# Optimization experiments

Measured on AMD Instinct MI355X. Metric: run time of the kernel, lower is better.

The kernel has to match this reference:

```python
import jax, jax.numpy as jnp
import numpy as np

DIM = 128
HEADS = 4
HEAD_DIM = DIM // HEADS
SCALE = HEAD_DIM ** -0.5


def setup_inputs() -> dict:
    k0 = jax.random.key(0)
    ks = jax.random.split(k0, 20)
    B, N, Hq, Wq_, Hk, Wk_ = 1, 6, 100, 100, 16, 44
    s = 0.02
    return {
        "query": jax.random.normal(ks[0], (B, DIM, Hq, Wq_), jnp.float32),
        "key": jax.random.normal(ks[1], (B, N, DIM, Hk, Wk_), jnp.float32),
        "value": jax.random.normal(ks[2], (B, N, DIM, Hk, Wk_), jnp.float32),
        "depth": jax.random.uniform(ks[3], (B, N, 1, Hk, Wk_), jnp.float32),
        "depth_confidence": jax.random.uniform(ks[4], (B, N, 1, Hk, Wk_), jnp.float32),
        "skip": jax.random.normal(ks[5], (B, DIM, Hq, Wq_), jnp.float32),
        "Wq": jax.random.normal(ks[6], (DIM, DIM), jnp.float32) * s,
        "bq": jnp.zeros((DIM,), jnp.float32),
        "Wk": jax.random.normal(ks[7], (DIM, DIM), jnp.float32) * s,
        "bk": jnp.zeros((DIM,), jnp.float32),
        "Wv": jax.random.normal(ks[8], (DIM, DIM), jnp.float32) * s,
        "bv": jnp.zeros((DIM,), jnp.float32),
        "Wo": jax.random.normal(ks[9], (DIM, DIM), jnp.float32) * s,
        "bo": jnp.zeros((DIM,), jnp.float32),
        "dw1": jax.random.normal(ks[10], (DIM // 4, 1), jnp.float32) * s,  # 1x1 conv: 1 -> dim/4
        "db1": jnp.zeros((DIM // 4,), jnp.float32),
        "dw2": jax.random.normal(ks[11], (HEADS, DIM // 4), jnp.float32) * s,  # 1x1 conv: dim/4 -> heads
        "db2": jnp.zeros((HEADS,), jnp.float32),
    }


def _forward(query, key, value, depth, depth_confidence, skip,
             Wq, bq, Wk, bk, Wv, bv, Wo, bo, dw1, db1, dw2, db2):
    B, dim, Hq, Wq_ = query.shape
    N, Hk, Wk_ = key.shape[1], key.shape[3], key.shape[4]
    Lq, Lk = Hq * Wq_, N * Hk * Wk_

    # b d h w -> b (h w) d
    qf = jnp.transpose(query, (0, 2, 3, 1)).reshape(B, Lq, dim)
    # b n d h w -> b (n h w) d
    kf = jnp.transpose(key, (0, 1, 3, 4, 2)).reshape(B, Lk, dim)
    vf = jnp.transpose(value, (0, 1, 3, 4, 2)).reshape(B, Lk, dim)

    def heads(x, W, b):  # (B,L,dim) -> (B,H,L,hd)
        y = x @ W.T + b
        return jnp.transpose(y.reshape(B, -1, HEADS, HEAD_DIM), (0, 2, 1, 3))

    Q = heads(qf, Wq, bq)
    K = heads(kf, Wk, bk)
    V = heads(vf, Wv, bv)

    attn = jnp.einsum('bhqd,bhkd->bhqk', Q, K) * SCALE  # (B,H,Lq,Lk)

    # depth weighting bias: two 1x1 convs + softmax over heads channel
    d = jnp.transpose(depth, (0, 1, 3, 4, 2))  # (B,N,Hk,Wk,1)
    t = jax.nn.relu(d @ dw1.T + db1)            # (B,N,Hk,Wk,dim/4)
    t = t @ dw2.T + db2                          # (B,N,Hk,Wk,heads)
    dw = jax.nn.softmax(t, axis=-1)
    conf = jnp.transpose(depth_confidence, (0, 1, 3, 4, 2))  # (B,N,Hk,Wk,1)
    cw = conf * dw                               # (B,N,Hk,Wk,heads)
    bias = 0.1 * jnp.transpose(cw, (0, 4, 1, 2, 3)).reshape(B, HEADS, 1, Lk)

    attn = jax.nn.softmax(attn + bias, axis=-1)
    out = jnp.einsum('bhqk,bhkd->bhqd', attn, V)             # (B,H,Lq,hd)
    out = jnp.transpose(out, (0, 2, 1, 3)).reshape(B, Lq, dim)
    out = out @ Wo.T + bo
    out = jnp.transpose(out.reshape(B, Hq, Wq_, dim), (0, 3, 1, 2))
    return out + skip


def reference(query, key, value, depth, depth_confidence, skip,
              Wq, bq, Wk, bk, Wv, bv, Wo, bo, dw1, db1, dw2, db2):
    return _forward(query, key, value, depth, depth_confidence, skip,
                    Wq, bq, Wk, bk, Wv, bv, Wo, bo, dw1, db1, dw2, db2)
```

## Files before the change

kernel.cpp:

```cpp
#include <hip/hip_runtime.h>
#include <stdint.h>

#define LQ 10000
#define LK 4224
#define NQB 313
#define SCALE 0.17677669529663687f
#define LOG2E 1.44269504088896341f
#define SCALE2 (SCALE * LOG2E)

typedef __bf16 bf16x8 __attribute__((ext_vector_type(8)));
typedef __bf16 bf16x4 __attribute__((ext_vector_type(4)));
typedef float  f32x4  __attribute__((ext_vector_type(4)));
typedef unsigned short u16x4 __attribute__((ext_vector_type(4)));

__device__ __forceinline__ unsigned short f2b(float f) {
  union { float f; unsigned u; } v; v.f = f;
  unsigned r = v.u + 0x7fffu + ((v.u >> 16) & 1u);
  return (unsigned short)(r >> 16);
}

__global__ void misc_kernel(
    const float* __restrict__ depth, const float* __restrict__ conf,
    const float* __restrict__ dw1, const float* __restrict__ db1,
    const float* __restrict__ dw2, const float* __restrict__ db2,
    const float* __restrict__ Wq, const float* __restrict__ Wk,
    const float* __restrict__ Wv, const float* __restrict__ Wo,
    float* __restrict__ biasArr,
    unsigned short* __restrict__ Wqb, unsigned short* __restrict__ Wkb,
    unsigned short* __restrict__ Wvb, unsigned short* __restrict__ Wob) {
  int b = blockIdx.x, t = threadIdx.x;
  if (b < 256) {
    int i = b * 256 + t;
    int m = i >> 14, j = i & 16383;
    const float* src = (m == 0) ? Wq : (m == 1) ? Wk : (m == 2) ? Wv : Wo;
    unsigned short* dst = (m == 0) ? Wqb : (m == 1) ? Wkb : (m == 2) ? Wvb : Wob;
    dst[j] = f2b(src[j]);
    return;
  }
  int k = (b - 256) * 256 + t;
  if (k >= LK) return;
  float d = depth[k], c = conf[k];
  float t2[4];
#pragma unroll
  for (int hh = 0; hh < 4; ++hh) t2[hh] = db2[hh];
  for (int cc = 0; cc < 32; ++cc) {
    float t1 = fmaxf(fmaf(d, dw1[cc], db1[cc]), 0.f);
#pragma unroll
    for (int hh = 0; hh < 4; ++hh) t2[hh] = fmaf(t1, dw2[hh * 32 + cc], t2[hh]);
  }
  float mx = fmaxf(fmaxf(t2[0], t2[1]), fmaxf(t2[2], t2[3]));
  float e[4], s = 0.f;
#pragma unroll
  for (int hh = 0; hh < 4; ++hh) { e[hh] = __expf(t2[hh] - mx); s += e[hh]; }
  float f = 0.1f * c / s * LOG2E;
#pragma unroll
  for (int hh = 0; hh < 4; ++hh) biasArr[hh * LK + k] = f * e[hh];
}

__global__ __launch_bounds__(256) void proj_kernel(
    const float* __restrict__ query, const float* __restrict__ key,
    const float* __restrict__ value,
    const unsigned short* __restrict__ Wqb, const float* __restrict__ bq,
    const unsigned short* __restrict__ Wkb, const float* __restrict__ bk,
    const unsigned short* __restrict__ Wvb, const float* __restrict__ bv,
    unsigned short* __restrict__ Qb, unsigned short* __restrict__ Kb,
    unsigned short* __restrict__ Vt) {
  __shared__ __align__(16) unsigned short Xb[64][136];
  int t = threadIdx.x;
  int bid = blockIdx.x;
  int isQ = (bid < 157);
  int kvid = bid - 157;
  int isV = (kvid >= 66);
  if (isV) kvid -= 66;

  const unsigned short* Wb = isQ ? Wqb : (isV ? Wvb : Wkb);
  const float* bb = isQ ? bq : (isV ? bv : bk);

  if (isQ) {
    int l0 = bid * 64;
#pragma unroll
    for (int i = 0; i < 32; ++i) {
      int e = t + 256 * i;
      int d = e >> 6, c = e & 63;
      int l = l0 + c;
      Xb[c][d] = f2b(l < LQ ? query[(size_t)d * LQ + l] : 0.f);
    }
  } else {
    const float* X = isV ? value : key;
    int k0 = kvid * 64;
    int n = k0 / 704, p0 = k0 % 704;
    const float* Xn = X + (size_t)n * 128 * 704 + p0;
#pragma unroll
    for (int i = 0; i < 32; ++i) {
      int e = t + 256 * i;
      int d = e >> 6, c = e & 63;
      Xb[c][d] = f2b(Xn[(size_t)d * 704 + c]);
    }
  }
  __syncthreads();
  int wv = t >> 6, lane = t & 63, lm = lane & 15, lg = lane >> 4;
  const f32x4 zf = {0.f, 0.f, 0.f, 0.f};
  bf16x8 af[4];
#pragma unroll
  for (int kk = 0; kk < 4; ++kk)
    af[kk] = *(const bf16x8*)&Xb[wv * 16 + lm][kk * 32 + lg * 8];
  f32x4 acc[8] = {zf, zf, zf, zf, zf, zf, zf, zf};
#pragma unroll
  for (int kk = 0; kk < 4; ++kk)
#pragma unroll
    for (int ni = 0; ni < 8; ++ni) {
      bf16x8 bfr = *(const bf16x8*)(Wb + (size_t)(ni * 16 + lm) * 128 + kk * 32 + lg * 8);
      acc[ni] = __builtin_amdgcn_mfma_f32_16x16x32_bf16(af[kk], bfr, acc[ni], 0, 0, 0);
    }
  if (isQ) {
    int l0 = bid * 64;
#pragma unroll
    for (int ni = 0; ni < 8; ++ni)
#pragma unroll
      for (int r = 0; r < 4; ++r) {
        int l = l0 + wv * 16 + lg * 4 + r;
        int dout = ni * 16 + lm;
        Qb[(size_t)l * 128 + dout] = f2b((acc[ni][r] + bb[dout]) * SCALE2);
      }
  } else if (!isV) {
    int k0 = kvid * 64;
#pragma unroll
    for (int ni = 0; ni < 8; ++ni)
#pragma unroll
      for (int r = 0; r < 4; ++r) {
        int k = k0 + wv * 16 + lg * 4 + r;
        int dout = ni * 16 + lm;
        Kb[(size_t)k * 128 + dout] = f2b(acc[ni][r] + bb[dout]);
      }
  } else {
    int k0 = kvid * 64;
#pragma unroll
    for (int ni = 0; ni < 8; ++ni)
#pragma unroll
      for (int r = 0; r < 4; ++r) {
        int k = k0 + wv * 16 + lg * 4 + r;
        int dout = ni * 16 + lm;
        Vt[(size_t)dout * LK + k] = f2b(acc[ni][r] + bb[dout]);
      }
  }
}

__global__ __launch_bounds__(256) void attn_part_kernel(
    const unsigned short* __restrict__ Qb, const unsigned short* __restrict__ Kb,
    const unsigned short* __restrict__ Vt, const float* __restrict__ biasArr,
    float* __restrict__ Opart, float* __restrict__ Ml, int tpc, int C) {
  __shared__ __align__(16) unsigned short P_lds[4][32][64];
  int t = threadIdx.x;
  int wv = t >> 6;
  int qb = blockIdx.x * 4 + wv;
  if (qb >= NQB) return;
  int h = blockIdx.y, c = blockIdx.z;
  int lane = t & 63, lm = lane & 15, lg = lane >> 4;
  const f32x4 zf = {0.f, 0.f, 0.f, 0.f};

  bf16x8 qf[2];
#pragma unroll
  for (int mi = 0; mi < 2; ++mi)
    qf[mi] = *(const bf16x8*)(Qb + (size_t)(qb * 32 + mi * 16 + lm) * 128 + h * 32 + lg * 8);

  f32x4 acc[2][2] = {{zf, zf}, {zf, zf}};
  float lrun[2] = {0.f, 0.f};

  const float* bias_h = biasArr + h * LK;
  const unsigned short* Kh = Kb + h * 32;
  const unsigned short* Vh = Vt + (size_t)h * 32 * LK;

  int wr_half = (lg & 1) * 4;
  int swz = lm & 7;

  int kb_end = c * tpc + tpc;
  for (int kb = c * tpc; kb < kb_end; ++kb) {
    int k0 = kb * 64;
    bf16x8 kf[4];
#pragma unroll
    for (int ni = 0; ni < 4; ++ni)
      kf[ni] = *(const bf16x8*)(Kh + (size_t)(k0 + ni * 16 + lm) * 128 + lg * 8);
    f32x4 bvv[4];
#pragma unroll
    for (int ni = 0; ni < 4; ++ni)
      bvv[ni] = *(const f32x4*)(bias_h + k0 + ni * 16 + lg * 4);

#pragma unroll
    for (int mi = 0; mi < 2; ++mi) {
      f32x4 S[4];
#pragma unroll
      for (int ni = 0; ni < 4; ++ni)
        S[ni] = __builtin_amdgcn_mfma_f32_16x16x32_bf16(kf[ni], qf[mi], zf, 0, 0, 0);
      float ps[4];
#pragma unroll
      for (int ni = 0; ni < 4; ++ni) {
        bf16x4 pk;
        float p0 = exp2f(S[ni][0] + bvv[ni][0]);
        float p1 = exp2f(S[ni][1] + bvv[ni][1]);
        float p2 = exp2f(S[ni][2] + bvv[ni][2]);
        float p3 = exp2f(S[ni][3] + bvv[ni][3]);
        pk[0] = (__bf16)p0; pk[1] = (__bf16)p1;
        pk[2] = (__bf16)p2; pk[3] = (__bf16)p3;
        ps[ni] = (p0 + p1) + (p2 + p3);
        int chunk = (2 * ni + (lg >> 1)) ^ swz;
        *(bf16x4*)&P_lds[wv][mi * 16 + lm][chunk * 8 + wr_half] = pk;
      }
      float psum = (ps[0] + ps[1]) + (ps[2] + ps[3]);
      psum += __shfl_xor(psum, 16);
      psum += __shfl_xor(psum, 32);
      lrun[mi] += psum;
    }
    asm volatile("" ::: "memory");
    __builtin_amdgcn_sched_barrier(0);
    bf16x8 pa[2][2], vfr[2][2];
#pragma unroll
    for (int mi = 0; mi < 2; ++mi)
#pragma unroll
      for (int kk = 0; kk < 2; ++kk) {
        int chunk = (4 * kk + lg) ^ swz;
        pa[mi][kk] = *(const bf16x8*)&P_lds[wv][mi * 16 + lm][chunk * 8];
      }
#pragma unroll
    for (int kk = 0; kk < 2; ++kk)
#pragma unroll
      for (int nd = 0; nd < 2; ++nd)
        vfr[kk][nd] = *(const bf16x8*)(Vh + (size_t)(nd * 16 + lm) * LK + k0 + kk * 32 + lg * 8);
#pragma unroll
    for (int mi = 0; mi < 2; ++mi)
#pragma unroll
      for (int nd = 0; nd < 2; ++nd)
#pragma unroll
        for (int kk = 0; kk < 2; ++kk)
          acc[mi][nd] = __builtin_amdgcn_mfma_f32_16x16x32_bf16(pa[mi][kk], vfr[kk][nd], acc[mi][nd], 0, 0, 0);
    asm volatile("" ::: "memory");
    __builtin_amdgcn_sched_barrier(0);
  }
  size_t pbase = (size_t)(qb * 4 + h) * C + c;
  float* Op = Opart + pbase * 1024;
#pragma unroll
  for (int mi = 0; mi < 2; ++mi)
#pragma unroll
    for (int nd = 0; nd < 2; ++nd)
#pragma unroll
      for (int r = 0; r < 4; ++r)
        Op[(mi * 16 + lg * 4 + r) * 32 + nd * 16 + lm] = acc[mi][nd][r];
  if (lane < 16) {
    float* MlB = Ml + pbase * 64;
#pragma unroll
    for (int mi = 0; mi < 2; ++mi)
      MlB[mi * 16 + lm] = lrun[mi];
  }
}

__global__ __launch_bounds__(256) void epi_kernel(
    const float* __restrict__ Opart, const float* __restrict__ Ml,
    const unsigned short* __restrict__ Wob, const float* __restrict__ bo,
    const float* __restrict__ skip, float* __restrict__ out, int C) {
  __shared__ __align__(16) unsigned short ObT[64][136];
  __shared__ float wls[4][32];
  int t = threadIdx.x, wv = t >> 6, lane = t & 63;
  int bx = blockIdx.x, l0 = bx * 64;
  int h = wv;

#pragma unroll
  for (int s = 0; s < 2; ++s) {
    int qb = bx * 2 + s;
    if (qb < NQB) {
      size_t base = (size_t)(qb * 4 + h) * C;
      if (lane < 32) {
        float lt = 0.f;
        for (int c = 0; c < C; ++c)
          lt += Ml[(base + c) * 64 + lane];
        wls[wv][lane] = 1.f / lt;
      }
      asm volatile("" ::: "memory");
      __builtin_amdgcn_sched_barrier(0);
      const float* Op = Opart + base * 1024;
#pragma unroll
      for (int j = 0; j < 4; ++j) {
        int q = j * 8 + (lane >> 3);
        int d = (lane & 7) * 4;
        f32x4 accv = {0.f, 0.f, 0.f, 0.f};
        for (int c = 0; c < C; ++c) {
          f32x4 v = *(const f32x4*)(Op + c * 1024 + j * 256 + lane * 4);
#pragma unroll
          for (int i = 0; i < 4; ++i) accv[i] += v[i];
        }
        float linv = wls[wv][q];
        u16x4 o4;
#pragma unroll
        for (int i = 0; i < 4; ++i) o4[i] = f2b(accv[i] * linv);
        *(u16x4*)&ObT[s * 32 + q][h * 32 + d] = o4;
      }
    } else {
#pragma unroll
      for (int j = 0; j < 4; ++j) {
        int q = j * 8 + (lane >> 3);
        int d = (lane & 7) * 4;
        u16x4 z = {0, 0, 0, 0};
        *(u16x4*)&ObT[s * 32 + q][h * 32 + d] = z;
      }
    }
  }
  __syncthreads();

  int lm = lane & 15, lg = lane >> 4;
  const f32x4 zf = {0.f, 0.f, 0.f, 0.f};
  bf16x8 af[2][4];
#pragma unroll
  for (int mi = 0; mi < 2; ++mi)
#pragma unroll
    for (int kk = 0; kk < 4; ++kk)
      af[mi][kk] = *(const bf16x8*)(Wob + (size_t)(wv * 32 + mi * 16 + lm) * 128 + kk * 32 + lg * 8);
  f32x4 acc[2][4] = {{zf, zf, zf, zf}, {zf, zf, zf, zf}};
#pragma unroll
  for (int kk = 0; kk < 4; ++kk) {
    bf16x8 bfr[4];
#pragma unroll
    for (int ni = 0; ni < 4; ++ni)
      bfr[ni] = *(const bf16x8*)&ObT[ni * 16 + lm][kk * 32 + lg * 8];
#pragma unroll
    for (int mi = 0; mi < 2; ++mi)
#pragma unroll
      for (int ni = 0; ni < 4; ++ni)
        acc[mi][ni] = __builtin_amdgcn_mfma_f32_16x16x32_bf16(af[mi][kk], bfr[ni], acc[mi][ni], 0, 0, 0);
  }
#pragma unroll
  for (int mi = 0; mi < 2; ++mi)
#pragma unroll
    for (int r = 0; r < 4; ++r) {
      int dout = wv * 32 + mi * 16 + lg * 4 + r;
      float bb = bo[dout];
#pragma unroll
      for (int ni = 0; ni < 4; ++ni) {
        int l = l0 + ni * 16 + lm;
        if (l < LQ)
          out[(size_t)dout * LQ + l] = acc[mi][ni][r] + bb + skip[(size_t)dout * LQ + l];
      }
    }
}

extern "C" void kernel_launch(void* const* d_in, const int* in_sizes, int n_in,
                              void* d_out, int out_size, void* d_ws, size_t ws_size,
                              hipStream_t stream) {
  const float* query = (const float*)d_in[0];
  const float* key   = (const float*)d_in[1];
  const float* value = (const float*)d_in[2];
  const float* depth = (const float*)d_in[3];
  const float* conf  = (const float*)d_in[4];
  const float* skip  = (const float*)d_in[5];
  const float* Wq = (const float*)d_in[6];   const float* bq = (const float*)d_in[7];
  const float* Wk = (const float*)d_in[8];   const float* bk = (const float*)d_in[9];
  const float* Wv = (const float*)d_in[10];  const float* bv = (const float*)d_in[11];
  const float* Wo = (const float*)d_in[12];  const float* bo = (const float*)d_in[13];
  const float* dw1 = (const float*)d_in[14]; const float* db1 = (const float*)d_in[15];
  const float* dw2 = (const float*)d_in[16]; const float* db2 = (const float*)d_in[17];
  float* out = (float*)d_out;
  char* ws = (char*)d_ws;

  unsigned short* Qb   = (unsigned short*)(ws + 0);
  unsigned short* Kb   = (unsigned short*)(ws + 2572288);
  unsigned short* Vt   = (unsigned short*)(ws + 3653632);
  float*          bias = (float*)        (ws + 4734976);
  unsigned short* Wqb  = (unsigned short*)(ws + 4802560);
  unsigned short* Wkb  = (unsigned short*)(ws + 4835328);
  unsigned short* Wvb  = (unsigned short*)(ws + 4868096);
  unsigned short* Wob  = (unsigned short*)(ws + 4900864);
  const size_t splitOff = 7505920;

  int C = 1;
  {
    const int cand[4] = {6, 3, 2, 1};
    for (int i = 0; i < 4; ++i) {
      size_t need = splitOff + (size_t)NQB * 4 * cand[i] * (4096 + 256);
      if (ws_size >= need) { C = cand[i]; break; }
    }
  }
  int tpc = 66 / C;
  float* Opart = (float*)(ws + splitOff);
  float* Ml    = (float*)(ws + splitOff + (size_t)NQB * 4 * C * 4096);

  hipLaunchKernelGGL(misc_kernel, dim3(273), dim3(256), 0, stream,
                     depth, conf, dw1, db1, dw2, db2, Wq, Wk, Wv, Wo,
                     bias, Wqb, Wkb, Wvb, Wob);
  hipLaunchKernelGGL(proj_kernel, dim3(289), dim3(256), 0, stream,
                     query, key, value, Wqb, bq, Wkb, bk, Wvb, bv, Qb, Kb, Vt);
  hipLaunchKernelGGL(attn_part_kernel, dim3(79, 4, C), dim3(256), 0, stream,
                     Qb, Kb, Vt, bias, Opart, Ml, tpc, C);
  hipLaunchKernelGGL(epi_kernel, dim3(157), dim3(256), 0, stream,
                     Opart, Ml, Wob, bo, skip, out, C);
}
```

Before: 239.2 us.

## Split each 32-row query block across two waves in attention kernel

Each wave now handles 16 query rows instead of 32, with two waves sharing one query block, and the grid doubles in x. This halves per-wave registers and LDS and raises wave-level parallelism, but each K/V tile is loaded twice as often per query row and per-wave MFMA reuse of K/V fragments drops. The sched_barrier fences between the score and PV stages are also removed, giving the compiler more freedom to interleave them.

```diff
diff --git a/kernel.cpp b/kernel.cpp
--- a/kernel.cpp
+++ b/kernel.cpp
@@ -149,22 +149,20 @@
     const unsigned short* __restrict__ Qb, const unsigned short* __restrict__ Kb,
     const unsigned short* __restrict__ Vt, const float* __restrict__ biasArr,
     float* __restrict__ Opart, float* __restrict__ Ml, int tpc, int C) {
-  __shared__ __align__(16) unsigned short P_lds[4][32][64];
+  __shared__ __align__(16) unsigned short P_lds[4][16][64];
   int t = threadIdx.x;
   int wv = t >> 6;
-  int qb = blockIdx.x * 4 + wv;
+  int qh = wv & 1;
+  int qb = blockIdx.x * 2 + (wv >> 1);
   if (qb >= NQB) return;
   int h = blockIdx.y, c = blockIdx.z;
   int lane = t & 63, lm = lane & 15, lg = lane >> 4;
   const f32x4 zf = {0.f, 0.f, 0.f, 0.f};
 
-  bf16x8 qf[2];
-#pragma unroll
-  for (int mi = 0; mi < 2; ++mi)
-    qf[mi] = *(const bf16x8*)(Qb + (size_t)(qb * 32 + mi * 16 + lm) * 128 + h * 32 + lg * 8);
-
-  f32x4 acc[2][2] = {{zf, zf}, {zf, zf}};
-  float lrun[2] = {0.f, 0.f};
+  bf16x8 qf = *(const bf16x8*)(Qb + (size_t)(qb * 32 + qh * 16 + lm) * 128 + h * 32 + lg * 8);
+
+  f32x4 acc[2] = {zf, zf};
+  float lrun = 0.f;
 
   const float* bias_h = biasArr + h * LK;
   const unsigned short* Kh = Kb + h * 32;
@@ -185,71 +183,55 @@
     for (int ni = 0; ni < 4; ++ni)
       bvv[ni] = *(const f32x4*)(bias_h + k0 + ni * 16 + lg * 4);
 
-#pragma unroll
-    for (int mi = 0; mi < 2; ++mi) {
-      f32x4 S[4];
-#pragma unroll
-      for (int ni = 0; ni < 4; ++ni)
-        S[ni] = __builtin_amdgcn_mfma_f32_16x16x32_bf16(kf[ni], qf[mi], zf, 0, 0, 0);
-      float ps[4];
-#pragma unroll
-      for (int ni = 0; ni < 4; ++ni) {
-        bf16x4 pk;
-        float p0 = exp2f(S[ni][0] + bvv[ni][0]);
-        float p1 = exp2f(S[ni][1] + bvv[ni][1]);
-        float p2 = exp2f(S[ni][2] + bvv[ni][2]);
-        float p3 = exp2f(S[ni][3] + bvv[ni][3]);
-        pk[0] = (__bf16)p0; pk[1] = (__bf16)p1;
-        pk[2] = (__bf16)p2; pk[3] = (__bf16)p3;
-        ps[ni] = (p0 + p1) + (p2 + p3);
-        int chunk = (2 * ni + (lg >> 1)) ^ swz;
-        *(bf16x4*)&P_lds[wv][mi * 16 + lm][chunk * 8 + wr_half] = pk;
-      }
-      float psum = (ps[0] + ps[1]) + (ps[2] + ps[3]);
-      psum += __shfl_xor(psum, 16);
-      psum += __shfl_xor(psum, 32);
-      lrun[mi] += psum;
-    }
-    asm volatile("" ::: "memory");
-    __builtin_amdgcn_sched_barrier(0);
-    bf16x8 pa[2][2], vfr[2][2];
-#pragma unroll
-    for (int mi = 0; mi < 2; ++mi)
-#pragma unroll
-      for (int kk = 0; kk < 2; ++kk) {
-        int chunk = (4 * kk + lg) ^ swz;
-        pa[mi][kk] = *(const bf16x8*)&P_lds[wv][mi * 16 + lm][chunk * 8];
-      }
+    f32x4 S[4];
+#pragma unroll
+    for (int ni = 0; ni < 4; ++ni)
+      S[ni] = __builtin_amdgcn_mfma_f32_16x16x32_bf16(kf[ni], qf, zf, 0, 0, 0);
+    float ps[4];
+#pragma unroll
+    for (int ni = 0; ni < 4; ++ni) {
+      bf16x4 pk;
+      float p0 = exp2f(S[ni][0] + bvv[ni][0]);
+      float p1 = exp2f(S[ni][1] + bvv[ni][1]);
+      float p2 = exp2f(S[ni][2] + bvv[ni][2]);
+      float p3 = exp2f(S[ni][3] + bvv[ni][3]);
+      pk[0] = (__bf16)p0; pk[1] = (__bf16)p1;
+      pk[2] = (__bf16)p2; pk[3] = (__bf16)p3;
+      ps[ni] = (p0 + p1) + (p2 + p3);
+      int chunk = (2 * ni + (lg >> 1)) ^ swz;
+      *(bf16x4*)&P_lds[wv][lm][chunk * 8 + wr_half] = pk;
+    }
+    float psum = (ps[0] + ps[1]) + (ps[2] + ps[3]);
+    psum += __shfl_xor(psum, 16);
+    psum += __shfl_xor(psum, 32);
+    lrun += psum;
+
+    bf16x8 pa[2], vfr[2][2];
+#pragma unroll
+    for (int kk = 0; kk < 2; ++kk) {
+      int chunk = (4 * kk + lg) ^ swz;
+      pa[kk] = *(const bf16x8*)&P_lds[wv][lm][chunk * 8];
+    }
 #pragma unroll
     for (int kk = 0; kk < 2; ++kk)
 #pragma unroll
       for (int nd = 0; nd < 2; ++nd)
         vfr[kk][nd] = *(const bf16x8*)(Vh + (size_t)(nd * 16 + lm) * LK + k0 + kk * 32 + lg * 8);
 #pragma unroll
-    for (int mi = 0; mi < 2; ++mi)
-#pragma unroll
-      for (int nd = 0; nd < 2; ++nd)
-#pragma unroll
-        for (int kk = 0; kk < 2; ++kk)
-          acc[mi][nd] = __builtin_amdgcn_mfma_f32_16x16x32_bf16(pa[mi][kk], vfr[kk][nd], acc[mi][nd], 0, 0, 0);
-    asm volatile("" ::: "memory");
-    __builtin_amdgcn_sched_barrier(0);
+    for (int nd = 0; nd < 2; ++nd)
+#pragma unroll
+      for (int kk = 0; kk < 2; ++kk)
+        acc[nd] = __builtin_amdgcn_mfma_f32_16x16x32_bf16(pa[kk], vfr[kk][nd], acc[nd], 0, 0, 0);
   }
   size_t pbase = (size_t)(qb * 4 + h) * C + c;
   float* Op = Opart + pbase * 1024;
 #pragma unroll
-  for (int mi = 0; mi < 2; ++mi)
-#pragma unroll
-    for (int nd = 0; nd < 2; ++nd)
-#pragma unroll
-      for (int r = 0; r < 4; ++r)
-        Op[(mi * 16 + lg * 4 + r) * 32 + nd * 16 + lm] = acc[mi][nd][r];
-  if (lane < 16) {
-    float* MlB = Ml + pbase * 64;
-#pragma unroll
-    for (int mi = 0; mi < 2; ++mi)
-      MlB[mi * 16 + lm] = lrun[mi];
-  }
+  for (int nd = 0; nd < 2; ++nd)
+#pragma unroll
+    for (int r = 0; r < 4; ++r)
+      Op[(qh * 16 + lg * 4 + r) * 32 + nd * 16 + lm] = acc[nd][r];
+  if (lane < 16)
+    Ml[pbase * 64 + qh * 16 + lm] = lrun;
 }
 
 __global__ __launch_bounds__(256) void epi_kernel(
@@ -385,7 +367,7 @@
                      bias, Wqb, Wkb, Wvb, Wob);
   hipLaunchKernelGGL(proj_kernel, dim3(289), dim3(256), 0, stream,
                      query, key, value, Wqb, bq, Wkb, bk, Wvb, bv, Qb, Kb, Vt);
-  hipLaunchKernelGGL(attn_part_kernel, dim3(79, 4, C), dim3(256), 0, stream,
+  hipLaunchKernelGGL(attn_part_kernel, dim3(157, 4, C), dim3(256), 0, stream,
                      Qb, Kb, Vt, bias, Opart, Ml, tpc, C);
   hipLaunchKernelGGL(epi_kernel, dim3(157), dim3(256), 0, stream,
                      Opart, Ml, Wob, bo, skip, out, C);
```

New measurement: 320.2 us. 33.9% more time.
